# Kernel optimization log

Measured on AMD Instinct MI355X. Metric: run time of the kernel, lower is better.

## Reference

```python
import jax, jax.numpy as jnp
import numpy as np

HASH_BUCKETS = 1024
D_MODEL = 256


def setup_inputs() -> dict:
    key = jax.random.key(0)
    ks = jax.random.split(key, 12)
    batch_a, batch_b, n_keys, d = 4096, 8192, 4, D_MODEL
    inp = {
        "table_a_emb": jax.random.normal(ks[0], (batch_a, d), dtype=jnp.float32),
        "table_b_emb": jax.random.normal(ks[1], (batch_b, d), dtype=jnp.float32),
        "keys_a": jax.random.randint(ks[2], (batch_a, n_keys), 0, 1000000, dtype=jnp.int64) if jax.config.jax_enable_x64 else jax.random.randint(ks[2], (batch_a, n_keys), 0, 1000000, dtype=jnp.int32),
        "keys_b": jax.random.randint(ks[3], (batch_b, n_keys), 0, 1000000, dtype=jnp.int64) if jax.config.jax_enable_x64 else jax.random.randint(ks[3], (batch_b, n_keys), 0, 1000000, dtype=jnp.int32),
        # SimpleMLP(d_in=2d, d_hidden=2d, n_hidden=1, d_out=d): in->hidden ReLU, hidden->out
        "W1": jax.random.normal(ks[4], (2 * d, 2 * d), dtype=jnp.float32) * (1.0 / np.sqrt(2 * d)),
        "b1": jnp.zeros((2 * d,), dtype=jnp.float32),
        "W2": jax.random.normal(ks[5], (2 * d, d), dtype=jnp.float32) * (1.0 / np.sqrt(2 * d)),
        "b2": jnp.zeros((d,), dtype=jnp.float32),
        "Wo": jax.random.normal(ks[6], (d, d), dtype=jnp.float32) * (1.0 / np.sqrt(d)),
        "bo": jnp.zeros((d,), dtype=jnp.float32),
    }
    return inp


def reference(table_a_emb, table_b_emb, keys_a, keys_b, W1, b1, W2, b2, Wo, bo):
    # hash-bucket matching: row i of table_a matches all rows of table_b with equal hash
    hash_a = jnp.sum(keys_a, axis=1) % HASH_BUCKETS  # (batch_a,)
    hash_b = jnp.sum(keys_b, axis=1) % HASH_BUCKETS  # (batch_b,)
    mask = (hash_a[:, None] == hash_b[None, :]).astype(table_b_emb.dtype)  # (batch_a, batch_b)
    count = mask.sum(axis=1, keepdims=True)  # (batch_a, 1)
    # mean of matched table_b embeddings; zeros when no match (matches torch loop semantics)
    agg_b = (mask @ table_b_emb) / jnp.maximum(count, 1.0)  # (batch_a, d)
    combined = jnp.concatenate([table_a_emb, agg_b], axis=-1)  # (batch_a, 2d)
    h = jax.nn.relu(combined @ W1 + b1)
    rel = h @ W2 + b2
    return rel @ Wo + bo
```

## Files before the change

kernel.cpp:

```cpp
#include <hip/hip_runtime.h>
#include <hip/hip_bf16.h>

#define HASH_BUCKETS 1024
#define BA 4096
#define BB 8192

typedef __attribute__((ext_vector_type(8))) short bf16x8;
typedef __attribute__((ext_vector_type(4))) float f32x4;

__device__ __forceinline__ short f2bf(float x) {
    union { float f; unsigned int u; } c;
    c.f = x;
    unsigned int lsb = (c.u >> 16) & 1u;
    c.u += 0x7fffu + lsb;
    return (short)(c.u >> 16);
}

__device__ __forceinline__ void gl_lds16(const void* g, void* l) {
    __builtin_amdgcn_global_load_lds((const __attribute__((address_space(1))) void*)g,
                                     (__attribute__((address_space(3))) void*)l, 16, 0, 0);
}

__global__ __launch_bounds__(256) void prep_kernel(
    const float* __restrict__ W1, const float* __restrict__ Wo,
    const float* __restrict__ W2, const float* __restrict__ b2,
    const float* __restrict__ bo, const float* __restrict__ ta,
    const float* __restrict__ tb, const int* __restrict__ ka,
    const int* __restrict__ kb, short* __restrict__ W1T,
    short* __restrict__ w2woT, short* __restrict__ tab,
    int* __restrict__ ha, float* __restrict__ bfused,
    short* __restrict__ bmean) {
    __shared__ __align__(16) char smem[36896];
    const int blk = blockIdx.x;
    const int t = threadIdx.x;
    if (blk < 64) {
        float(*tl)[65] = (float(*)[65])smem;
        const int tr = (blk >> 3) * 64, tc = (blk & 7) * 64;
        const int c = t & 63, r0 = t >> 6;
#pragma unroll
        for (int i = 0; i < 16; ++i) {
            int r = r0 + i * 4;
            tl[r][c] = W1[(size_t)(tr + r) * 512 + tc + c];
        }
        __syncthreads();
#pragma unroll
        for (int i = 0; i < 16; ++i) {
            int r = r0 + i * 4;
            W1T[(size_t)(tc + r) * 512 + tr + c] = f2bf(tl[c][r]);
        }
    } else if (blk < 96) {
        float* As = (float*)smem;
        float* Bs = (float*)(smem + 8704);
        const int b = blk - 64;
        const int bn = (b & 3) * 64;
        const int bm = (b >> 2) * 64;
        const int tx = t & 15, ty = t >> 4;
        float acc[4][4] = {};
        for (int c0 = 0; c0 < 256; c0 += 32) {
            {
                const int cc = t & 31, mb = t >> 5;
#pragma unroll
                for (int mi = 0; mi < 8; ++mi) {
                    int m = mi * 8 + mb;
                    As[cc * 68 + m] = W2[(size_t)(bm + m) * 256 + c0 + cc];
                }
            }
            {
                const int nn = t & 63, cb = t >> 6;
#pragma unroll
                for (int ci = 0; ci < 8; ++ci) {
                    int c = ci * 4 + cb;
                    Bs[c * 68 + nn] = Wo[(size_t)(c0 + c) * 256 + bn + nn];
                }
            }
            __syncthreads();
#pragma unroll
            for (int cc = 0; cc < 32; ++cc) {
                float4 a = *(const float4*)&As[cc * 68 + ty * 4];
                float4 bv = *(const float4*)&Bs[cc * 68 + tx * 4];
                acc[0][0] += a.x * bv.x; acc[0][1] += a.x * bv.y; acc[0][2] += a.x * bv.z; acc[0][3] += a.x * bv.w;
                acc[1][0] += a.y * bv.x; acc[1][1] += a.y * bv.y; acc[1][2] += a.y * bv.z; acc[1][3] += a.y * bv.w;
                acc[2][0] += a.z * bv.x; acc[2][1] += a.z * bv.y; acc[2][2] += a.z * bv.z; acc[2][3] += a.z * bv.w;
                acc[3][0] += a.w * bv.x; acc[3][1] += a.w * bv.y; acc[3][2] += a.w * bv.z; acc[3][3] += a.w * bv.w;
            }
            __syncthreads();
        }
#pragma unroll
        for (int r = 0; r < 4; ++r)
#pragma unroll
            for (int c = 0; c < 4; ++c) {
                int k = bm + ty * 4 + r, n = bn + tx * 4 + c;
                w2woT[(size_t)n * 512 + k] = f2bf(acc[r][c]);
            }
    } else if (blk < 160) {
        const int b = blk - 96;
#pragma unroll
        for (int i = 0; i < 16; ++i) {
            int e = b * 4096 + i * 256 + t;
            float4 v = ((const float4*)ta)[e];
            short4 s;
            s.x = f2bf(v.x); s.y = f2bf(v.y); s.z = f2bf(v.z); s.w = f2bf(v.w);
            ((short4*)tab)[e] = s;
        }
    } else if (blk < 176) {
        const int r = (blk - 160) * 256 + t;
        int4 k4 = ((const int4*)ka)[r];
        ha[r] = (k4.x + k4.y + k4.z + k4.w) & (HASH_BUCKETS - 1);
    } else if (blk == 176) {
        float acc = bo[t];
        for (int k = 0; k < 256; ++k) acc += b2[k] * Wo[(size_t)k * 256 + t];
        bfused[t] = acc;
    } else {
        int* sh = (int*)smem;
        float* part = (float*)(smem + 32768);
        int* pcnt = (int*)(smem + 36864);
        const int h = blk - 177;
        const int w = t >> 6, l = t & 63;
#pragma unroll 4
        for (int i = 0; i < 32; ++i) {
            int r = i * 256 + t;
            int4 k4 = ((const int4*)kb)[r];
            sh[r] = (k4.x + k4.y + k4.z + k4.w) & (HASH_BUCKETS - 1);
        }
        __syncthreads();
        float a0 = 0.f, a1 = 0.f, a2 = 0.f, a3 = 0.f;
        int cnt = 0;
#pragma unroll 4
        for (int it = 0; it < 32; ++it) {
            int base = w * 2048 + it * 64;
            unsigned long long m = __ballot(sh[base + l] == h);
            cnt += __popcll(m);
            while (m) {
                int j = base + (__ffsll((long long)m) - 1);
                m &= (m - 1);
                const float* row = tb + (size_t)j * 256;
                a0 += row[l];
                a1 += row[l + 64];
                a2 += row[l + 128];
                a3 += row[l + 192];
            }
        }
        part[w * 256 + l] = a0;
        part[w * 256 + l + 64] = a1;
        part[w * 256 + l + 128] = a2;
        part[w * 256 + l + 192] = a3;
        if (l == 0) pcnt[w] = cnt;
        __syncthreads();
        float s = part[t] + part[256 + t] + part[512 + t] + part[768 + t];
        int c = pcnt[0] + pcnt[1] + pcnt[2] + pcnt[3];
        bmean[(size_t)h * 256 + t] = f2bf(s / (float)max(c, 1));
    }
}

template <int MODE>
__global__ __launch_bounds__(256) void mfgemm(const short* __restrict__ A,
                                              const short* __restrict__ Bt,
                                              const short* __restrict__ tab,
                                              const short* __restrict__ bmean,
                                              const int* __restrict__ ha,
                                              const float* __restrict__ bias,
                                              void* __restrict__ Cv,
                                              int M, int N, int K) {
    __shared__ short As[2][64 * 64];
    __shared__ short Bs[2][64 * 64];
    const int tid = threadIdx.x;
    const int l = tid & 63, w = tid >> 6;
    const int wm = w >> 1, wn = w & 1;
    const int bm = blockIdx.y * 64, bn = blockIdx.x * 64;

    const int r0 = (w * 2 + 0) * 8 + (l >> 3);
    const int r1 = (w * 2 + 1) * 8 + (l >> 3);
    const int sk0 = ((l & 7) ^ (r0 & 7)) * 8;
    const int sk1 = ((l & 7) ^ (r1 & 7)) * 8;
    const int arow0 = bm + r0, arow1 = bm + r1;
    const int brow0 = bn + r0, brow1 = bn + r1;
    int ha0 = 0, ha1 = 0;
    if (MODE == 0) { ha0 = ha[arow0]; ha1 = ha[arow1]; }
    const int dst0 = (w * 2 + 0) * 512;
    const int dst1 = (w * 2 + 1) * 512;

    const int lr = l & 15;
    const int g = l >> 4;
    f32x4 acc[2][2] = {};

    auto STAGE = [&](int nb, int kt) {
        const int k0 = kt * 64;
        const short *as0, *as1;
        if (MODE == 0) {
            if (k0 < 256) {
                as0 = &tab[(size_t)arow0 * 256 + k0 + sk0];
                as1 = &tab[(size_t)arow1 * 256 + k0 + sk1];
            } else {
                as0 = &bmean[(size_t)ha0 * 256 + (k0 - 256) + sk0];
                as1 = &bmean[(size_t)ha1 * 256 + (k0 - 256) + sk1];
            }
        } else {
            as0 = &A[(size_t)arow0 * K + k0 + sk0];
            as1 = &A[(size_t)arow1 * K + k0 + sk1];
        }
        gl_lds16(as0, &As[nb][dst0]);
        gl_lds16(as1, &As[nb][dst1]);
        gl_lds16(&Bt[(size_t)brow0 * K + k0 + sk0], &Bs[nb][dst0]);
        gl_lds16(&Bt[(size_t)brow1 * K + k0 + sk1], &Bs[nb][dst1]);
    };

    auto COMPUTE = [&](int nb) {
        const short* ab = &As[nb][0];
        const short* bb = &Bs[nb][0];
        bf16x8 af[2][2], bfr[2][2];
#pragma unroll
        for (int mf = 0; mf < 2; ++mf) {
            const int rr = wm * 32 + mf * 16 + lr;
#pragma unroll
            for (int ks = 0; ks < 2; ++ks)
                af[mf][ks] = *(const bf16x8*)&ab[rr * 64 + (((ks * 4 + g) ^ (lr & 7)) * 8)];
        }
#pragma unroll
        for (int nf = 0; nf < 2; ++nf) {
            const int rr = wn * 32 + nf * 16 + lr;
#pragma unroll
            for (int ks = 0; ks < 2; ++ks)
                bfr[nf][ks] = *(const bf16x8*)&bb[rr * 64 + (((ks * 4 + g) ^ (lr & 7)) * 8)];
        }
#pragma unroll
        for (int ks = 0; ks < 2; ++ks)
#pragma unroll
            for (int mf = 0; mf < 2; ++mf)
#pragma unroll
                for (int nf = 0; nf < 2; ++nf)
                    acc[mf][nf] = __builtin_amdgcn_mfma_f32_16x16x32_bf16(
                        af[mf][ks], bfr[nf][ks], acc[mf][nf], 0, 0, 0);
    };

    const int nt = K >> 6;
    STAGE(0, 0);
    asm volatile("s_waitcnt vmcnt(0)" ::: "memory");
    __syncthreads();
    for (int t = 0; t < nt; ++t) {
        const int cur = t & 1;
        if (t + 1 < nt) STAGE(cur ^ 1, t + 1);
        COMPUTE(cur);
        asm volatile("s_waitcnt vmcnt(0)" ::: "memory");
        __syncthreads();
    }

#pragma unroll
    for (int mf = 0; mf < 2; ++mf)
#pragma unroll
        for (int nf = 0; nf < 2; ++nf) {
            const int col = bn + wn * 32 + nf * 16 + lr;
            const int rbase = bm + wm * 32 + mf * 16 + ((l >> 4) << 2);
            const float bv = bias[col];
#pragma unroll
            for (int i = 0; i < 4; ++i) {
                const float x = acc[mf][nf][i] + bv;
                const int row = rbase + i;
                if (MODE == 0)
                    ((short*)Cv)[(size_t)row * N + col] = f2bf(fmaxf(x, 0.f));
                else
                    ((float*)Cv)[(size_t)row * N + col] = x;
            }
        }
}

extern "C" void kernel_launch(void* const* d_in, const int* in_sizes, int n_in,
                              void* d_out, int out_size, void* d_ws, size_t ws_size,
                              hipStream_t stream) {
    const float* ta = (const float*)d_in[0];
    const float* tb = (const float*)d_in[1];
    const int* ka = (const int*)d_in[2];
    const int* kb = (const int*)d_in[3];
    const float* W1 = (const float*)d_in[4];
    const float* b1 = (const float*)d_in[5];
    const float* W2 = (const float*)d_in[6];
    const float* b2 = (const float*)d_in[7];
    const float* Wo = (const float*)d_in[8];
    const float* bo = (const float*)d_in[9];
    float* out = (float*)d_out;

    char* ws = (char*)d_ws;
    int* ha = (int*)(ws + 0);
    short* bmean = (short*)(ws + 16384);
    short* tab = (short*)(ws + 540672);
    short* W1T = (short*)(ws + 2637824);
    short* w2woT = (short*)(ws + 3162112);
    float* bfused = (float*)(ws + 3424256);
    short* hbuf = (short*)(ws + 3425280);

    prep_kernel<<<1201, 256, 0, stream>>>(W1, Wo, W2, b2, bo, ta, tb, ka, kb,
                                          W1T, w2woT, tab, ha, bfused, bmean);
    mfgemm<0><<<dim3(8, 64), 256, 0, stream>>>(nullptr, W1T, tab, bmean, ha, b1,
                                               hbuf, BA, 512, 512);
    mfgemm<1><<<dim3(4, 64), 256, 0, stream>>>(hbuf, w2woT, nullptr, nullptr, nullptr,
                                               bfused, out, BA, 256, 512);
}
```

Before: 35.44 us.

## Move W2·Wo fusion from scalar prep blocks into MFMA tiles of first GEMM

The prep kernel no longer computes W2@Wo with FP32 scalar FMAs in 32 blocks. It now only transposes Wo and converts W2 to bf16. The fused weight product is computed by extra MFMA tiles appended to the first GEMM launch, which write w2woT transposed for the second GEMM. This shortens the critical prep stage and overlaps the small weight GEMM with the main hidden-layer GEMM. The cost is extra workspace, bf16 rounding of W2 and Wo before multiplication, and an uncoalesced transposed store in the new mode.

```diff
diff --git a/kernel.cpp b/kernel.cpp
--- a/kernel.cpp
+++ b/kernel.cpp
@@ -27,9 +27,9 @@
     const float* __restrict__ bo, const float* __restrict__ ta,
     const float* __restrict__ tb, const int* __restrict__ ka,
     const int* __restrict__ kb, short* __restrict__ W1T,
-    short* __restrict__ w2woT, short* __restrict__ tab,
-    int* __restrict__ ha, float* __restrict__ bfused,
-    short* __restrict__ bmean) {
+    short* __restrict__ WoT, short* __restrict__ W2b,
+    short* __restrict__ tab, int* __restrict__ ha,
+    float* __restrict__ bfused, short* __restrict__ bmean) {
     __shared__ __align__(16) char smem[36896];
     const int blk = blockIdx.x;
     const int t = threadIdx.x;
@@ -48,52 +48,34 @@
             int r = r0 + i * 4;
             W1T[(size_t)(tc + r) * 512 + tr + c] = f2bf(tl[c][r]);
         }
-    } else if (blk < 96) {
-        float* As = (float*)smem;
-        float* Bs = (float*)(smem + 8704);
+    } else if (blk < 80) {
+        float(*tl)[65] = (float(*)[65])smem;
         const int b = blk - 64;
-        const int bn = (b & 3) * 64;
-        const int bm = (b >> 2) * 64;
-        const int tx = t & 15, ty = t >> 4;
-        float acc[4][4] = {};
-        for (int c0 = 0; c0 < 256; c0 += 32) {
-            {
-                const int cc = t & 31, mb = t >> 5;
-#pragma unroll
-                for (int mi = 0; mi < 8; ++mi) {
-                    int m = mi * 8 + mb;
-                    As[cc * 68 + m] = W2[(size_t)(bm + m) * 256 + c0 + cc];
-                }
-            }
-            {
-                const int nn = t & 63, cb = t >> 6;
-#pragma unroll
-                for (int ci = 0; ci < 8; ++ci) {
-                    int c = ci * 4 + cb;
-                    Bs[c * 68 + nn] = Wo[(size_t)(c0 + c) * 256 + bn + nn];
-                }
-            }
-            __syncthreads();
-#pragma unroll
-            for (int cc = 0; cc < 32; ++cc) {
-                float4 a = *(const float4*)&As[cc * 68 + ty * 4];
-                float4 bv = *(const float4*)&Bs[cc * 68 + tx * 4];
-                acc[0][0] += a.x * bv.x; acc[0][1] += a.x * bv.y; acc[0][2] += a.x * bv.z; acc[0][3] += a.x * bv.w;
-                acc[1][0] += a.y * bv.x; acc[1][1] += a.y * bv.y; acc[1][2] += a.y * bv.z; acc[1][3] += a.y * bv.w;
-                acc[2][0] += a.z * bv.x; acc[2][1] += a.z * bv.y; acc[2][2] += a.z * bv.z; acc[2][3] += a.z * bv.w;
-                acc[3][0] += a.w * bv.x; acc[3][1] += a.w * bv.y; acc[3][2] += a.w * bv.z; acc[3][3] += a.w * bv.w;
-            }
-            __syncthreads();
-        }
-#pragma unroll
-        for (int r = 0; r < 4; ++r)
-#pragma unroll
-            for (int c = 0; c < 4; ++c) {
-                int k = bm + ty * 4 + r, n = bn + tx * 4 + c;
-                w2woT[(size_t)n * 512 + k] = f2bf(acc[r][c]);
-            }
-    } else if (blk < 160) {
-        const int b = blk - 96;
+        const int tr = (b >> 2) * 64, tc = (b & 3) * 64;
+        const int c = t & 63, r0 = t >> 6;
+#pragma unroll
+        for (int i = 0; i < 16; ++i) {
+            int r = r0 + i * 4;
+            tl[r][c] = Wo[(size_t)(tr + r) * 256 + tc + c];
+        }
+        __syncthreads();
+#pragma unroll
+        for (int i = 0; i < 16; ++i) {
+            int r = r0 + i * 4;
+            WoT[(size_t)(tc + r) * 256 + tr + c] = f2bf(tl[c][r]);
+        }
+    } else if (blk < 88) {
+        const int g = (blk - 80) * 256 + t;
+#pragma unroll
+        for (int i = 0; i < 16; ++i) {
+            int e = g + i * 2048;
+            float4 v = ((const float4*)W2)[e];
+            short4 s;
+            s.x = f2bf(v.x); s.y = f2bf(v.y); s.z = f2bf(v.z); s.w = f2bf(v.w);
+            ((short4*)W2b)[e] = s;
+        }
+    } else if (blk < 152) {
+        const int b = blk - 88;
 #pragma unroll
         for (int i = 0; i < 16; ++i) {
             int e = b * 4096 + i * 256 + t;
@@ -102,11 +84,11 @@
             s.x = f2bf(v.x); s.y = f2bf(v.y); s.z = f2bf(v.z); s.w = f2bf(v.w);
             ((short4*)tab)[e] = s;
         }
-    } else if (blk < 176) {
-        const int r = (blk - 160) * 256 + t;
+    } else if (blk < 168) {
+        const int r = (blk - 152) * 256 + t;
         int4 k4 = ((const int4*)ka)[r];
         ha[r] = (k4.x + k4.y + k4.z + k4.w) & (HASH_BUCKETS - 1);
-    } else if (blk == 176) {
+    } else if (blk == 168) {
         float acc = bo[t];
         for (int k = 0; k < 256; ++k) acc += b2[k] * Wo[(size_t)k * 256 + t];
         bfused[t] = acc;
@@ -114,7 +96,7 @@
         int* sh = (int*)smem;
         float* part = (float*)(smem + 32768);
         int* pcnt = (int*)(smem + 36864);
-        const int h = blk - 177;
+        const int h = blk - 169;
         const int w = t >> 6, l = t & 63;
 #pragma unroll 4
         for (int i = 0; i < 32; ++i) {
@@ -153,20 +135,18 @@
 }
 
 template <int MODE>
-__global__ __launch_bounds__(256) void mfgemm(const short* __restrict__ A,
-                                              const short* __restrict__ Bt,
-                                              const short* __restrict__ tab,
-                                              const short* __restrict__ bmean,
-                                              const int* __restrict__ ha,
-                                              const float* __restrict__ bias,
-                                              void* __restrict__ Cv,
-                                              int M, int N, int K) {
-    __shared__ short As[2][64 * 64];
-    __shared__ short Bs[2][64 * 64];
+__device__ __forceinline__ void gemm_tile(short* __restrict__ As, short* __restrict__ Bs,
+                                          const short* __restrict__ A,
+                                          const short* __restrict__ Bt,
+                                          const short* __restrict__ tab,
+                                          const short* __restrict__ bmean,
+                                          const int* __restrict__ ha,
+                                          const float* __restrict__ bias,
+                                          void* __restrict__ Cv,
+                                          int bm, int bn, int M, int N, int K) {
     const int tid = threadIdx.x;
     const int l = tid & 63, w = tid >> 6;
     const int wm = w >> 1, wn = w & 1;
-    const int bm = blockIdx.y * 64, bn = blockIdx.x * 64;
 
     const int r0 = (w * 2 + 0) * 8 + (l >> 3);
     const int r1 = (w * 2 + 1) * 8 + (l >> 3);
@@ -198,15 +178,15 @@
             as0 = &A[(size_t)arow0 * K + k0 + sk0];
             as1 = &A[(size_t)arow1 * K + k0 + sk1];
         }
-        gl_lds16(as0, &As[nb][dst0]);
-        gl_lds16(as1, &As[nb][dst1]);
-        gl_lds16(&Bt[(size_t)brow0 * K + k0 + sk0], &Bs[nb][dst0]);
-        gl_lds16(&Bt[(size_t)brow1 * K + k0 + sk1], &Bs[nb][dst1]);
+        gl_lds16(as0, As + nb * 4096 + dst0);
+        gl_lds16(as1, As + nb * 4096 + dst1);
+        gl_lds16(&Bt[(size_t)brow0 * K + k0 + sk0], Bs + nb * 4096 + dst0);
+        gl_lds16(&Bt[(size_t)brow1 * K + k0 + sk1], Bs + nb * 4096 + dst1);
     };
 
     auto COMPUTE = [&](int nb) {
-        const short* ab = &As[nb][0];
-        const short* bb = &Bs[nb][0];
+        const short* ab = As + nb * 4096;
+        const short* bb = Bs + nb * 4096;
         bf16x8 af[2][2], bfr[2][2];
 #pragma unroll
         for (int mf = 0; mf < 2; ++mf) {
@@ -250,17 +230,49 @@
         for (int nf = 0; nf < 2; ++nf) {
             const int col = bn + wn * 32 + nf * 16 + lr;
             const int rbase = bm + wm * 32 + mf * 16 + ((l >> 4) << 2);
-            const float bv = bias[col];
+            float bv = 0.f;
+            if (MODE < 2) bv = bias[col];
 #pragma unroll
             for (int i = 0; i < 4; ++i) {
                 const float x = acc[mf][nf][i] + bv;
                 const int row = rbase + i;
                 if (MODE == 0)
                     ((short*)Cv)[(size_t)row * N + col] = f2bf(fmaxf(x, 0.f));
+                else if (MODE == 1)
+                    ((float*)Cv)[(size_t)row * N + col] = x;
                 else
-                    ((float*)Cv)[(size_t)row * N + col] = x;
+                    ((short*)Cv)[(size_t)col * M + row] = f2bf(x);
             }
         }
+}
+
+__global__ __launch_bounds__(256) void g1_kernel(const short* __restrict__ W1T,
+                                                 const short* __restrict__ tab,
+                                                 const short* __restrict__ bmean,
+                                                 const int* __restrict__ ha,
+                                                 const float* __restrict__ b1,
+                                                 short* __restrict__ hbuf,
+                                                 const short* __restrict__ W2b,
+                                                 const short* __restrict__ WoT,
+                                                 short* __restrict__ w2woT) {
+    __shared__ short As[2 * 4096];
+    __shared__ short Bs[2 * 4096];
+    if (blockIdx.y < 64)
+        gemm_tile<0>(As, Bs, nullptr, W1T, tab, bmean, ha, b1, hbuf,
+                     blockIdx.y * 64, blockIdx.x * 64, BA, 512, 512);
+    else
+        gemm_tile<2>(As, Bs, W2b, WoT, nullptr, nullptr, nullptr, nullptr, w2woT,
+                     blockIdx.x * 64, (blockIdx.y - 64) * 64, 512, 256, 256);
+}
+
+__global__ __launch_bounds__(256) void g2_kernel(const short* __restrict__ hbuf,
+                                                 const short* __restrict__ w2woT,
+                                                 const float* __restrict__ bfused,
+                                                 float* __restrict__ out) {
+    __shared__ short As[2 * 4096];
+    __shared__ short Bs[2 * 4096];
+    gemm_tile<1>(As, Bs, hbuf, w2woT, nullptr, nullptr, nullptr, bfused, out,
+                 blockIdx.y * 64, blockIdx.x * 64, BA, 256, 512);
 }
 
 extern "C" void kernel_launch(void* const* d_in, const int* in_sizes, int n_in,
@@ -286,11 +298,12 @@
     short* w2woT = (short*)(ws + 3162112);
     float* bfused = (float*)(ws + 3424256);
     short* hbuf = (short*)(ws + 3425280);
-
-    prep_kernel<<<1201, 256, 0, stream>>>(W1, Wo, W2, b2, bo, ta, tb, ka, kb,
-                                          W1T, w2woT, tab, ha, bfused, bmean);
-    mfgemm<0><<<dim3(8, 64), 256, 0, stream>>>(nullptr, W1T, tab, bmean, ha, b1,
-                                               hbuf, BA, 512, 512);
-    mfgemm<1><<<dim3(4, 64), 256, 0, stream>>>(hbuf, w2woT, nullptr, nullptr, nullptr,
-                                               bfused, out, BA, 256, 512);
-}
+    short* WoT = (short*)(ws + 7619584);
+    short* W2b = (short*)(ws + 7750656);
+
+    prep_kernel<<<1193, 256, 0, stream>>>(W1, Wo, W2, b2, bo, ta, tb, ka, kb,
+                                          W1T, WoT, W2b, tab, ha, bfused, bmean);
+    g1_kernel<<<dim3(8, 68), 256, 0, stream>>>(W1T, tab, bmean, ha, b1, hbuf,
+                                               W2b, WoT, w2woT);
+    g2_kernel<<<dim3(4, 64), 256, 0, stream>>>(hbuf, w2woT, bfused, out);
+}
```

Measured after the change: 34.76 us, median of 2. No clear change (-1.9%).
